# Optimization experiments

Measured on AMD Instinct MI355X. Metric: run time of the kernel, lower is better.

Reference implementation:

```python
import jax, jax.numpy as jnp
import numpy as np

EPS = 1e-6

def setup_inputs() -> dict:
    key = jax.random.key(0)
    k1, k2, k3 = jax.random.split(key, 3)
    B, N, C = 128, 196, 1024  # B = b*f = 8*16
    x = jax.random.normal(k1, (B, N, C), dtype=jnp.float32)
    w_qkv = jax.random.normal(k2, (3 * C, C), dtype=jnp.float32) * (C ** -0.5)
    w_proj = jax.random.normal(k3, (C, C), dtype=jnp.float32) * (C ** -0.5)
    b_proj = jnp.zeros((C,), dtype=jnp.float32)
    return {"x": x, "w_qkv": w_qkv, "w_proj": w_proj, "b_proj": b_proj, "num_frames": 16}

def reference(x, w_qkv, w_proj, b_proj, num_frames):
    B, N, C = x.shape
    H = 16
    e = C // H
    scale = e ** -0.5
    f = num_frames
    b = B // f
    # qkv projection (no bias), split k-first per rearrange 'b n (k c) -> k b n c'
    qkv = jnp.einsum('bnc,dc->bnd', x, w_qkv)          # [B, N, 3C]
    qkv = qkv.reshape(B, N, 3, H, e)
    q, k, v = qkv[:, :, 0], qkv[:, :, 1], qkv[:, :, 2]  # [B, N, H, e]
    # relu feature map + scale offset
    q_ = jax.nn.relu(q) + scale
    k_ = jax.nn.relu(k) + scale
    # fold frames into the token axis per video: [b, f*n, H, e]
    L = f * N
    q_ = q_.reshape(b, L, H, e)
    k_ = k_.reshape(b, L, H, e)
    v_ = v.reshape(b, L, H, e)
    # linear attention: kv accumulation [b, H, e, e]
    kv = jnp.einsum('bnhe,bnhd->bhed', k_, v_)
    k_sum = jnp.sum(k_, axis=1, keepdims=True)          # [b, 1, H, e]
    z = 1.0 / (jnp.sum(q_ * k_sum, axis=-1) + EPS)       # [b, L, H]
    out = jnp.einsum('bnhe,bhed->bnhd', q_, kv) * z[..., None]  # [b, L, H, e]
    out = out.reshape(B, N, C)
    return jnp.einsum('bnc,dc->bnd', out, w_proj) + b_proj
```

## Files before the change

kernel.cpp:

```cpp
#include <hip/hip_runtime.h>
#include <hip/hip_bf16.h>
#include <stdint.h>

typedef __attribute__((ext_vector_type(8))) short bf16x8;
typedef __attribute__((ext_vector_type(4))) float f32x4;

__device__ __forceinline__ unsigned short f2bf(float f) {
    unsigned u = __builtin_bit_cast(unsigned, f);
    u += 0x7FFF + ((u >> 16) & 1);
    return (unsigned short)(u >> 16);
}
__device__ __forceinline__ float bf2f(unsigned short h) {
    return __builtin_bit_cast(float, (unsigned)h << 16);
}
__device__ __forceinline__ void load_lds16(const void* g, void* l) {
    __builtin_amdgcn_global_load_lds(
        (const __attribute__((address_space(1))) void*)g,
        (__attribute__((address_space(3))) void*)l, 16, 0, 0);
}

__global__ __launch_bounds__(256)
void cvt_kernel(const float* __restrict__ src, unsigned short* __restrict__ dst)
{
    const long i = ((long)blockIdx.x * 256 + threadIdx.x) * 8;
    const float4 a = *(const float4*)(src + i);
    const float4 b = *(const float4*)(src + i + 4);
    bf16x8 r;
    r[0] = (short)f2bf(a.x); r[1] = (short)f2bf(a.y);
    r[2] = (short)f2bf(a.z); r[3] = (short)f2bf(a.w);
    r[4] = (short)f2bf(b.x); r[5] = (short)f2bf(b.y);
    r[6] = (short)f2bf(b.z); r[7] = (short)f2bf(b.w);
    *(bf16x8*)(dst + i) = r;
}

template<int MODE>
__global__ __launch_bounds__(256, 2)
void gemm_bt_kernel(const unsigned short* __restrict__ A,
                    const unsigned short* __restrict__ Bt,
                    __hip_bfloat16* __restrict__ o0,
                    __hip_bfloat16* __restrict__ o1,
                    __hip_bfloat16* __restrict__ o2,
                    float* __restrict__ outf,
                    const float* __restrict__ bias)
{
    constexpr int K  = 1024;
    constexpr int NT = (MODE == 0) ? 24 : 8;
    __shared__ __attribute__((aligned(16))) unsigned short As[128 * 64];
    __shared__ __attribute__((aligned(16))) unsigned short Bs[128 * 64];

    const int bid   = blockIdx.x;
    const int npg   = 8 * NT;
    const int group = bid / npg;
    const int rem   = bid - group * npg;
    const int gm    = (196 - group * 8 < 8) ? (196 - group * 8) : 8;
    const int mt    = group * 8 + rem % gm;
    const int nt    = rem / gm;
    const long m0 = (long)mt * 128;
    const long n0 = (long)nt * 128;

    const int t    = threadIdx.x;
    const int lane = t & 63;
    const int wv   = t >> 6;
    const int wm   = (wv & 1) << 6;
    const int wn   = (wv >> 1) << 6;
    const int fr   = lane & 15;
    const int qd   = lane >> 4;

    f32x4 acc[4][4] = {};

    const int srow   = t >> 3;
    const int gch    = (t & 7) ^ (srow & 7);
    const int wbytes = (t & 192) << 4;

    const unsigned short* Ag = A  + (m0 + srow) * K + gch * 8;
    const unsigned short* Bg = Bt + (n0 + srow) * K + gch * 8;

    for (int kb = 0; kb < K; kb += 64) {
        __syncthreads();
#pragma unroll
        for (int c = 0; c < 4; ++c) {
            load_lds16(Ag + (long)c * 32 * K + kb, (char*)As + c * 4096 + wbytes);
            load_lds16(Bg + (long)c * 32 * K + kb, (char*)Bs + c * 4096 + wbytes);
        }
        __syncthreads();
#pragma unroll
        for (int s = 0; s < 2; ++s) {
            bf16x8 af[4], bfv[4];
            const int ch = ((s << 2) + qd) ^ (fr & 7);
#pragma unroll
            for (int i = 0; i < 4; ++i)
                af[i] = *(const bf16x8*)(As + (wm + i * 16 + fr) * 64 + ch * 8);
#pragma unroll
            for (int j = 0; j < 4; ++j)
                bfv[j] = *(const bf16x8*)(Bs + (wn + j * 16 + fr) * 64 + ch * 8);
#pragma unroll
            for (int i = 0; i < 4; ++i)
#pragma unroll
                for (int j = 0; j < 4; ++j)
                    acc[i][j] = __builtin_amdgcn_mfma_f32_16x16x32_bf16(
                        af[i], bfv[j], acc[i][j], 0, 0, 0);
        }
    }

    if (MODE == 0) {
        const int which = nt >> 3;
        __hip_bfloat16* dst = (which == 0) ? o0 : (which == 1) ? o1 : o2;
        const int colbase = ((nt & 7) << 7) + wn;
        const bool act = (which < 2);
#pragma unroll
        for (int i = 0; i < 4; ++i) {
            const long mrow = m0 + wm + i * 16 + qd * 4;
#pragma unroll
            for (int r = 0; r < 4; ++r) {
                const long moff = (mrow + r) * 1024;
#pragma unroll
                for (int j = 0; j < 4; ++j) {
                    float v = acc[i][j][r];
                    if (act) v = fmaxf(v, 0.f) + 0.125f;
                    dst[moff + colbase + j * 16 + fr] = __float2bfloat16(v);
                }
            }
        }
    } else {
        const long nbase = n0 + wn;
#pragma unroll
        for (int i = 0; i < 4; ++i) {
            const long mrow = m0 + wm + i * 16 + qd * 4;
#pragma unroll
            for (int r = 0; r < 4; ++r) {
                const long moff = (mrow + r) * 1024;
#pragma unroll
                for (int j = 0; j < 4; ++j)
                    outf[moff + nbase + j * 16 + fr] =
                        acc[i][j][r] + bias[nbase + j * 16 + fr];
            }
        }
    }
}

__global__ __launch_bounds__(256)
void kv_partial_kernel(const __hip_bfloat16* __restrict__ kbuf,
                       const __hip_bfloat16* __restrict__ vbuf,
                       float* __restrict__ kvp,
                       float* __restrict__ ksump)
{
    __shared__ float kf[8][512];
    __shared__ float vf[8][512];
    const int t   = threadIdx.x;
    const int bid = blockIdx.x;
    const int sp   = bid % 14;
    const int hoct = (bid / 14) & 1;
    const int bb   = bid / 28;
    const long rowstart = (long)bb * 3136 + sp * 224;

    const int hsub = t >> 5;
    const int w    = t & 31;
    const int E    = w >> 2;
    const int Dq   = w & 3;
    const int cb   = hsub * 64;
    const int e0   = cb + E * 8;
    const int d0   = cb + Dq * 16;

    float kvacc[8][16];
#pragma unroll
    for (int i = 0; i < 8; ++i)
#pragma unroll
        for (int j = 0; j < 16; ++j) kvacc[i][j] = 0.f;
    float ksacc[8] = {0, 0, 0, 0, 0, 0, 0, 0};

    for (int it = 0; it < 28; ++it) {
        __syncthreads();
#pragma unroll
        for (int i = 0; i < 4; ++i) {
            const int idx = t + (i << 8);
            const int rr  = (idx >> 6) & 7;
            const int c   = idx & 63;
            const long grow = rowstart + it * 8 + rr;
            const __hip_bfloat16* srcp =
                ((idx < 512) ? kbuf : vbuf) + grow * 1024 + hoct * 512 + c * 8;
            bf16x8 v8 = *(const bf16x8*)srcp;
            float* dstp = (idx < 512) ? &kf[rr][c * 8] : &vf[rr][c * 8];
#pragma unroll
            for (int jj = 0; jj < 8; ++jj)
                dstp[jj] = bf2f((unsigned short)v8[jj]);
        }
        __syncthreads();
#pragma unroll
        for (int r = 0; r < 8; ++r) {
            float ke[8], vd[16];
#pragma unroll
            for (int i = 0; i < 8; ++i)  ke[i] = kf[r][e0 + i];
#pragma unroll
            for (int j = 0; j < 16; ++j) vd[j] = vf[r][d0 + j];
#pragma unroll
            for (int i = 0; i < 8; ++i) {
                ksacc[i] += ke[i];
#pragma unroll
                for (int j = 0; j < 16; ++j)
                    kvacc[i][j] += ke[i] * vd[j];
            }
        }
    }

    const int bh = bb * 16 + hoct * 8 + hsub;
    const int s2 = E >> 2, qd = E & 3;
    float* outp = kvp + ((long)sp * 128 + bh) * 4096 + ((s2 * 4 + Dq) * 64 + qd * 16) * 8;
#pragma unroll
    for (int fr = 0; fr < 16; ++fr)
#pragma unroll
        for (int jj = 0; jj < 8; ++jj)
            outp[fr * 8 + jj] = kvacc[jj][fr];
    if (Dq == 0) {
#pragma unroll
        for (int i = 0; i < 8; ++i)
            ksump[sp * 8192 + bh * 64 + E * 8 + i] = ksacc[i];
    }
}

__global__ __launch_bounds__(256)
void reduce_kv_kernel(const float* __restrict__ kvp, const float* __restrict__ ksump,
                      unsigned short* __restrict__ kvb, float* __restrict__ ksum)
{
    const int idx = blockIdx.x * 256 + threadIdx.x;
    if (idx < 128 * 4096) {
        float a = 0.f;
#pragma unroll
        for (int s = 0; s < 14; ++s) a += kvp[(long)s * 128 * 4096 + idx];
        kvb[idx] = f2bf(a);
    } else {
        const int j = idx - 128 * 4096;
        if (j < 128 * 64) {
            float a = 0.f;
#pragma unroll
            for (int s = 0; s < 14; ++s) a += ksump[s * 8192 + j];
            ksum[j] = a;
        }
    }
}

__global__ __launch_bounds__(256)
void attn_out_kernel(const __hip_bfloat16* __restrict__ qbuf,
                     const unsigned short* __restrict__ kvb,
                     const float* __restrict__ ksum,
                     __hip_bfloat16* __restrict__ out2)
{
    __shared__ __attribute__((aligned(16))) unsigned short qs[64][64];
    __shared__ float kss[64];
    __shared__ float zs[64];
    const int t   = threadIdx.x;
    const int bid = blockIdx.x;
    const int mc  = bid % 49;
    const int h   = (bid / 49) & 15;
    const int bb  = bid / 784;
    const long bh = bb * 16 + h;
    const long mbase = (long)bb * 3136 + mc * 64;

#pragma unroll
    for (int i = 0; i < 2; ++i) {
        const int idx = t + (i << 8);
        const int row = idx >> 3;
        const int c   = idx & 7;
        *(bf16x8*)&qs[row][c * 8] =
            *(const bf16x8*)(qbuf + (mbase + row) * 1024 + h * 64 + c * 8);
    }
    if (t < 64) kss[t] = ksum[bh * 64 + t];
    __syncthreads();
    if (t < 64) {
        float p = 0.f;
#pragma unroll
        for (int e = 0; e < 64; ++e) p += bf2f(qs[t][e]) * kss[e];
        zs[t] = 1.f / (p + 1e-6f);
    }
    __syncthreads();

    const int lane = t & 63;
    const int wv   = t >> 6;
    const int fr   = lane & 15;
    const int qd   = lane >> 4;

    bf16x8 bfv[2][4];
#pragma unroll
    for (int s2 = 0; s2 < 2; ++s2)
#pragma unroll
        for (int j = 0; j < 4; ++j)
            bfv[s2][j] = *(const bf16x8*)(kvb + bh * 4096 + ((s2 * 4 + j) * 64 + lane) * 8);

    const bf16x8 af0 = *(const bf16x8*)&qs[wv * 16 + fr][qd * 8];
    const bf16x8 af1 = *(const bf16x8*)&qs[wv * 16 + fr][32 + qd * 8];

    float zr[4];
#pragma unroll
    for (int r = 0; r < 4; ++r) zr[r] = zs[wv * 16 + qd * 4 + r];

#pragma unroll
    for (int j = 0; j < 4; ++j) {
        f32x4 acc = {};
        acc = __builtin_amdgcn_mfma_f32_16x16x32_bf16(af0, bfv[0][j], acc, 0, 0, 0);
        acc = __builtin_amdgcn_mfma_f32_16x16x32_bf16(af1, bfv[1][j], acc, 0, 0, 0);
#pragma unroll
        for (int r = 0; r < 4; ++r) {
            const long m = mbase + wv * 16 + qd * 4 + r;
            out2[m * 1024 + h * 64 + j * 16 + fr] = __float2bfloat16(acc[r] * zr[r]);
        }
    }
}

extern "C" void kernel_launch(void* const* d_in, const int* in_sizes, int n_in,
                              void* d_out, int out_size, void* d_ws, size_t ws_size,
                              hipStream_t stream)
{
    const float* x      = (const float*)d_in[0];
    const float* w_qkv  = (const float*)d_in[1];
    const float* w_proj = (const float*)d_in[2];
    const float* b_proj = (const float*)d_in[3];
    float* out = (float*)d_out;

    const long M = 25088;
    char* ws = (char*)d_ws;
    size_t off = 0;
    auto alloc = [&](size_t bytes) {
        char* p = ws + off;
        off += (bytes + 255) & ~(size_t)255;
        return p;
    };
    char* xb_region = alloc(M * 1024 * 2);
    unsigned short* xb     = (unsigned short*)xb_region;
    float*          kvp    = (float*)xb_region;
    float*          ksump  = (float*)(xb_region + (size_t)14 * 128 * 4096 * 4);
    unsigned short* wqkvb  = (unsigned short*)alloc((size_t)3072 * 1024 * 2);
    unsigned short* wprojb = (unsigned short*)alloc((size_t)1024 * 1024 * 2);
    unsigned short* vbuf   = (unsigned short*)alloc(M * 1024 * 2);
    unsigned short* kvb    = (unsigned short*)alloc((size_t)128 * 4096 * 2);
    float*          ksumr  = (float*)alloc((size_t)128 * 64 * 4);
    __hip_bfloat16* qbuf = (__hip_bfloat16*)d_out;
    __hip_bfloat16* kbuf = qbuf + M * 1024;
    __hip_bfloat16* out2 = (__hip_bfloat16*)vbuf;

    cvt_kernel<<<12544, 256, 0, stream>>>(x, xb);
    cvt_kernel<<<1536, 256, 0, stream>>>(w_qkv, wqkvb);
    cvt_kernel<<<512, 256, 0, stream>>>(w_proj, wprojb);
    gemm_bt_kernel<0><<<196 * 24, 256, 0, stream>>>(
        xb, wqkvb, qbuf, kbuf, (__hip_bfloat16*)vbuf, nullptr, nullptr);
    kv_partial_kernel<<<224, 256, 0, stream>>>(kbuf, (const __hip_bfloat16*)vbuf, kvp, ksump);
    reduce_kv_kernel<<<2080, 256, 0, stream>>>(kvp, ksump, kvb, ksumr);
    attn_out_kernel<<<8 * 16 * 49, 256, 0, stream>>>(qbuf, kvb, ksumr, out2);
    gemm_bt_kernel<1><<<196 * 8, 256, 0, stream>>>(
        (const unsigned short*)out2, wprojb, nullptr, nullptr, nullptr, out, b_proj);
}
```

Baseline: 532.4 us.

## Rewrite GEMM as 256x256 tile, 8-wave, double-buffered pipelined kernel

Replaces the 128x128-tile, 4-wave GEMM with a 256x256-tile, 512-thread kernel. It double-buffers LDS with global_load_lds staging interleaved between MFMA phases, and uses explicit waitcnt, barriers and s_setprio scheduling. The intent is to hide global-load latency behind matrix math and to raise arithmetic intensity per tile. The cost is much larger LDS use (128KB), more accumulator registers, and fewer blocks (1176 and 392), which risks poor occupancy and tail effects on the projection GEMM.

```diff
diff --git a/kernel.cpp b/kernel.cpp
--- a/kernel.cpp
+++ b/kernel.cpp
@@ -33,8 +33,69 @@
     *(bf16x8*)(dst + i) = r;
 }
 
+#define LD_A(p, i, s) (*(const bf16x8*)&lds[p][wr][((i) * 16 + fr) * 64 + ((((s) << 2) + qd) ^ cx) * 8])
+#define LD_B(p, j, s) (*(const bf16x8*)&lds[p][2 + bh_][(brow_ + (j) * 16 + fr) * 64 + ((((s) << 2) + qd) ^ cx) * 8])
+
+#define LDA4(p, ib) do { \
+    afr[0][0] = LD_A(p, (ib)+0, 0); afr[0][1] = LD_A(p, (ib)+0, 1); \
+    afr[1][0] = LD_A(p, (ib)+1, 0); afr[1][1] = LD_A(p, (ib)+1, 1); \
+    afr[2][0] = LD_A(p, (ib)+2, 0); afr[2][1] = LD_A(p, (ib)+2, 1); \
+    afr[3][0] = LD_A(p, (ib)+3, 0); afr[3][1] = LD_A(p, (ib)+3, 1); \
+} while (0)
+
+#define LDB2(p, jb) do { \
+    bfr[(jb)+0][0] = LD_B(p, (jb)+0, 0); bfr[(jb)+0][1] = LD_B(p, (jb)+0, 1); \
+    bfr[(jb)+1][0] = LD_B(p, (jb)+1, 0); bfr[(jb)+1][1] = LD_B(p, (jb)+1, 1); \
+} while (0)
+
+#define STAGE_A(p, half, tile) do { \
+    const unsigned short* s_ = Ag + (long)((half) * 128) * 1024 + (tile) * 64; \
+    unsigned short* d_ = ldsw + ((p) * 4 + (half)) * 8192; \
+    load_lds16(s_, d_); \
+    load_lds16(s_ + (long)64 * 1024, d_ + 4096); \
+} while (0)
+
+#define STAGE_B(p, half, tile) do { \
+    const unsigned short* s_ = Bg + (long)((half) * 128) * 1024 + (tile) * 64; \
+    unsigned short* d_ = ldsw + ((p) * 4 + 2 + (half)) * 8192; \
+    load_lds16(s_, d_); \
+    load_lds16(s_ + (long)64 * 1024, d_ + 4096); \
+} while (0)
+
+#define MM(ib, jb) do { \
+    _Pragma("unroll") \
+    for (int i_ = 0; i_ < 4; ++i_) { \
+        acc[(ib)+i_][(jb)+0] = __builtin_amdgcn_mfma_f32_16x16x32_bf16(afr[i_][0], bfr[(jb)+0][0], acc[(ib)+i_][(jb)+0], 0, 0, 0); \
+        acc[(ib)+i_][(jb)+1] = __builtin_amdgcn_mfma_f32_16x16x32_bf16(afr[i_][0], bfr[(jb)+1][0], acc[(ib)+i_][(jb)+1], 0, 0, 0); \
+    } \
+    _Pragma("unroll") \
+    for (int i_ = 0; i_ < 4; ++i_) { \
+        acc[(ib)+i_][(jb)+0] = __builtin_amdgcn_mfma_f32_16x16x32_bf16(afr[i_][1], bfr[(jb)+0][1], acc[(ib)+i_][(jb)+0], 0, 0, 0); \
+        acc[(ib)+i_][(jb)+1] = __builtin_amdgcn_mfma_f32_16x16x32_bf16(afr[i_][1], bfr[(jb)+1][1], acc[(ib)+i_][(jb)+1], 0, 0, 0); \
+    } \
+} while (0)
+
+#define PH_MID() do { \
+    __builtin_amdgcn_sched_barrier(0); \
+    __builtin_amdgcn_s_barrier(); \
+    asm volatile("s_waitcnt lgkmcnt(0)" ::: "memory"); \
+    __builtin_amdgcn_sched_barrier(0); \
+    __builtin_amdgcn_s_setprio(1); \
+} while (0)
+
+#define PH_END() do { \
+    __builtin_amdgcn_s_setprio(0); \
+    __builtin_amdgcn_s_barrier(); \
+} while (0)
+
+#define PH_END_V(n) do { \
+    __builtin_amdgcn_s_setprio(0); \
+    asm volatile("s_waitcnt vmcnt(" #n ")" ::: "memory"); \
+    __builtin_amdgcn_s_barrier(); \
+} while (0)
+
 template<int MODE>
-__global__ __launch_bounds__(256, 2)
+__global__ __launch_bounds__(512, 2)
 void gemm_bt_kernel(const unsigned short* __restrict__ A,
                     const unsigned short* __restrict__ Bt,
                     __hip_bfloat16* __restrict__ o0,
@@ -44,72 +105,90 @@
                     const float* __restrict__ bias)
 {
     constexpr int K  = 1024;
-    constexpr int NT = (MODE == 0) ? 24 : 8;
-    __shared__ __attribute__((aligned(16))) unsigned short As[128 * 64];
-    __shared__ __attribute__((aligned(16))) unsigned short Bs[128 * 64];
+    constexpr int NT = (MODE == 0) ? 12 : 4;
+    __shared__ __attribute__((aligned(16))) unsigned short lds[2][4][8192];
 
     const int bid   = blockIdx.x;
     const int npg   = 8 * NT;
     const int group = bid / npg;
     const int rem   = bid - group * npg;
-    const int gm    = (196 - group * 8 < 8) ? (196 - group * 8) : 8;
+    const int gm    = (98 - group * 8 < 8) ? (98 - group * 8) : 8;
     const int mt    = group * 8 + rem % gm;
     const int nt    = rem / gm;
-    const long m0 = (long)mt * 128;
-    const long n0 = (long)nt * 128;
+    const long m0 = (long)mt * 256;
+    const long n0 = (long)nt * 256;
 
     const int t    = threadIdx.x;
     const int lane = t & 63;
     const int wv   = t >> 6;
-    const int wm   = (wv & 1) << 6;
-    const int wn   = (wv >> 1) << 6;
+    const int wr   = wv >> 2;
+    const int wc   = wv & 3;
     const int fr   = lane & 15;
     const int qd   = lane >> 4;
-
-    f32x4 acc[4][4] = {};
-
-    const int srow   = t >> 3;
-    const int gch    = (t & 7) ^ (srow & 7);
-    const int wbytes = (t & 192) << 4;
-
+    const int cx   = fr & 7;
+    const int bh_   = wc >> 1;
+    const int brow_ = (wc & 1) << 6;
+
+    const int srow = t >> 3;
+    const int gch  = (t & 7) ^ (srow & 7);
     const unsigned short* Ag = A  + (m0 + srow) * K + gch * 8;
     const unsigned short* Bg = Bt + (n0 + srow) * K + gch * 8;
-
-    for (int kb = 0; kb < K; kb += 64) {
-        __syncthreads();
-#pragma unroll
-        for (int c = 0; c < 4; ++c) {
-            load_lds16(Ag + (long)c * 32 * K + kb, (char*)As + c * 4096 + wbytes);
-            load_lds16(Bg + (long)c * 32 * K + kb, (char*)Bs + c * 4096 + wbytes);
-        }
-        __syncthreads();
-#pragma unroll
-        for (int s = 0; s < 2; ++s) {
-            bf16x8 af[4], bfv[4];
-            const int ch = ((s << 2) + qd) ^ (fr & 7);
-#pragma unroll
-            for (int i = 0; i < 4; ++i)
-                af[i] = *(const bf16x8*)(As + (wm + i * 16 + fr) * 64 + ch * 8);
-#pragma unroll
-            for (int j = 0; j < 4; ++j)
-                bfv[j] = *(const bf16x8*)(Bs + (wn + j * 16 + fr) * 64 + ch * 8);
-#pragma unroll
-            for (int i = 0; i < 4; ++i)
-#pragma unroll
-                for (int j = 0; j < 4; ++j)
-                    acc[i][j] = __builtin_amdgcn_mfma_f32_16x16x32_bf16(
-                        af[i], bfv[j], acc[i][j], 0, 0, 0);
-        }
-    }
+    unsigned short* const ldsw = &lds[0][0][0] + wv * 512;
+
+    f32x4 acc[8][4] = {};
+    bf16x8 afr[4][2], bfr[4][2];
+
+    STAGE_B(0, 0, 0); STAGE_B(0, 1, 0); STAGE_A(0, 0, 0); STAGE_A(0, 1, 0);
+    STAGE_B(1, 0, 1); STAGE_B(1, 1, 1);
+    asm volatile("s_waitcnt vmcnt(4)" ::: "memory");
+    __builtin_amdgcn_s_barrier();
+
+#pragma unroll 1
+    for (int it = 0; it < 7; ++it) {
+        const int t1 = 2 * it + 1, t2 = 2 * it + 2, t3 = 2 * it + 3;
+        LDA4(0, 0); LDB2(0, 0); STAGE_A(1, 0, t1);
+        PH_MID(); MM(0, 0); PH_END();
+        LDB2(0, 2); STAGE_A(1, 1, t1);
+        PH_MID(); MM(0, 2); PH_END();
+        LDA4(0, 4); STAGE_B(0, 0, t2);
+        PH_MID(); MM(4, 0); PH_END();
+        STAGE_B(0, 1, t2);
+        PH_MID(); MM(4, 2); PH_END_V(4);
+        LDA4(1, 0); LDB2(1, 0); STAGE_A(0, 0, t2);
+        PH_MID(); MM(0, 0); PH_END();
+        LDB2(1, 2); STAGE_A(0, 1, t2);
+        PH_MID(); MM(0, 2); PH_END();
+        LDA4(1, 4); STAGE_B(1, 0, t3);
+        PH_MID(); MM(4, 0); PH_END();
+        STAGE_B(1, 1, t3);
+        PH_MID(); MM(4, 2); PH_END_V(4);
+    }
+    LDA4(0, 0); LDB2(0, 0); STAGE_A(1, 0, 15);
+    PH_MID(); MM(0, 0); PH_END();
+    LDB2(0, 2); STAGE_A(1, 1, 15);
+    PH_MID(); MM(0, 2); PH_END();
+    LDA4(0, 4);
+    PH_MID(); MM(4, 0); PH_END();
+    PH_MID(); MM(4, 2); PH_END_V(0);
+    LDA4(1, 0); LDB2(1, 0);
+    PH_MID(); MM(0, 0); PH_END();
+    LDB2(1, 2);
+    PH_MID(); MM(0, 2); PH_END();
+    LDA4(1, 4);
+    PH_MID(); MM(4, 0); PH_END();
+    __builtin_amdgcn_s_barrier();
+    asm volatile("s_waitcnt lgkmcnt(0)" ::: "memory");
+    __builtin_amdgcn_sched_barrier(0);
+    __builtin_amdgcn_s_setprio(1); MM(4, 2); __builtin_amdgcn_s_setprio(0);
 
     if (MODE == 0) {
-        const int which = nt >> 3;
+        const int which = nt >> 2;
         __hip_bfloat16* dst = (which == 0) ? o0 : (which == 1) ? o1 : o2;
-        const int colbase = ((nt & 7) << 7) + wn;
+        const int colbase = ((nt & 3) << 8) + wc * 64;
         const bool act = (which < 2);
 #pragma unroll
-        for (int i = 0; i < 4; ++i) {
-            const long mrow = m0 + wm + i * 16 + qd * 4;
+        for (int i = 0; i < 8; ++i) {
+            const long mrow = m0 + wr * 128 + i * 16 + qd * 4;
 #pragma unroll
             for (int r = 0; r < 4; ++r) {
                 const long moff = (mrow + r) * 1024;
@@ -122,10 +201,10 @@
             }
         }
     } else {
-        const long nbase = n0 + wn;
-#pragma unroll
-        for (int i = 0; i < 4; ++i) {
-            const long mrow = m0 + wm + i * 16 + qd * 4;
+        const long nbase = n0 + wc * 64;
+#pragma unroll
+        for (int i = 0; i < 8; ++i) {
+            const long mrow = m0 + wr * 128 + i * 16 + qd * 4;
 #pragma unroll
             for (int r = 0; r < 4; ++r) {
                 const long moff = (mrow + r) * 1024;
@@ -339,11 +418,11 @@
     cvt_kernel<<<12544, 256, 0, stream>>>(x, xb);
     cvt_kernel<<<1536, 256, 0, stream>>>(w_qkv, wqkvb);
     cvt_kernel<<<512, 256, 0, stream>>>(w_proj, wprojb);
-    gemm_bt_kernel<0><<<196 * 24, 256, 0, stream>>>(
+    gemm_bt_kernel<0><<<98 * 12, 512, 0, stream>>>(
         xb, wqkvb, qbuf, kbuf, (__hip_bfloat16*)vbuf, nullptr, nullptr);
     kv_partial_kernel<<<224, 256, 0, stream>>>(kbuf, (const __hip_bfloat16*)vbuf, kvp, ksump);
     reduce_kv_kernel<<<2080, 256, 0, stream>>>(kvp, ksump, kvb, ksumr);
     attn_out_kernel<<<8 * 16 * 49, 256, 0, stream>>>(qbuf, kvb, ksumr, out2);
-    gemm_bt_kernel<1><<<196 * 8, 256, 0, stream>>>(
+    gemm_bt_kernel<1><<<98 * 4, 512, 0, stream>>>(
         (const unsigned short*)out2, wprojb, nullptr, nullptr, nullptr, out, b_proj);
 }
```

Measured after the change: 516.6 us. 3.0% less time.
